# Kernel tuning notes

Measured on AMD Instinct MI355X. Metric: run time of the kernel, lower is better.

Reference implementation:

```python
import jax, jax.numpy as jnp
import numpy as np

N = 40000          # nodes
E = 640000         # edges (avg degree 16)
D = 128            # in_channels == out_channels
G = 8              # graphs
NPG = N // G       # nodes per graph
EPS = 1e-6
SLOPE = 0.01       # torch LeakyReLU default


def leaky(x):
    return jnp.where(x >= 0, x, SLOPE * x)


def setup_inputs() -> dict:
    key = jax.random.key(0)
    ks = jax.random.split(key, 8)
    x = jax.random.normal(ks[0], (N, D), dtype=jnp.float32)
    edge_index = jax.random.randint(ks[1], (2, E), 0, N, dtype=jnp.int32)
    w = jax.random.uniform(ks[2], (E, 1), dtype=jnp.float32)
    batch = jnp.repeat(jnp.arange(G, dtype=jnp.int32), NPG)
    batch_num = jnp.full((G,), NPG, dtype=jnp.int32)
    s = 1.0 / np.sqrt(D)
    W1 = jax.random.uniform(ks[3], (D, D), jnp.float32, -s, s)
    W2 = jax.random.uniform(ks[4], (D, D), jnp.float32, -s, s)
    Wo = jax.random.uniform(ks[5], (D, D), jnp.float32, -s, s)
    Wn = jax.random.uniform(ks[6], (D, D), jnp.float32, -s, s)
    gamma = jnp.ones((D,), jnp.float32)
    beta = jnp.zeros((D,), jnp.float32)
    return {"x": x, "edge_index": edge_index, "w": w, "batch": batch,
            "batch_num": batch_num, "W1": W1, "W2": W2, "Wo": Wo, "Wn": Wn,
            "gamma": gamma, "beta": beta}


def reference(x, edge_index, w, batch, batch_num, W1, W2, Wo, Wn, gamma, beta):
    # mlp_x (dropout in eval mode => identity)
    h = leaky(x @ W1) @ W2                                    # [N, D]
    # gather -> scale -> scatter-sum -> activate
    xj = w * h[edge_index[1]]                                 # [E, D]
    xn = leaky(jax.ops.segment_sum(xj, edge_index[0], num_segments=N))
    out = h @ Wo + xn @ Wn                                    # [N, D]
    # GraphNorm: per-graph mean and unbiased std (torch_scatter defaults)
    cnt = batch_num.astype(jnp.float32)[:, None]              # [G, 1]
    mu = jax.ops.segment_sum(out, batch, num_segments=G) / cnt
    diff = out - mu[batch]
    var = jax.ops.segment_sum(diff * diff, batch, num_segments=G) / (cnt - 1.0)
    sigma = jnp.sqrt(var)
    return diff / (sigma[batch] + EPS) * gamma + beta
```

## Files before the change

kernel.cpp:

```cpp
#include <hip/hip_runtime.h>
#include <hip/hip_bf16.h>

#define D 128
#define NN 40000
#define EE 640000
#define GG 8
#define NPG 5000
#define CSUB 16
#define NBKT 8
#define OVCAP 4095
#define REP 32

using short8 = __attribute__((ext_vector_type(8))) short;
using f32x4 = __attribute__((ext_vector_type(4))) float;

__device__ __forceinline__ float lrelu(float v) { return v >= 0.f ? v : 0.01f * v; }

__device__ __forceinline__ ushort f2bf(float f) {
    union { float f; uint u; } c; c.f = f;
    return (ushort)((c.u + 0x7FFFu + ((c.u >> 16) & 1u)) >> 16);
}
__device__ __forceinline__ float bf2f_lo(uint u) { union { uint u; float f; } c; c.u = u << 16; return c.f; }
__device__ __forceinline__ float bf2f_hi(uint u) { union { uint u; float f; } c; c.u = u & 0xFFFF0000u; return c.f; }

__global__ __launch_bounds__(256) void prep_k(const float* __restrict__ W1,
                                              const float* __restrict__ W2,
                                              const float* __restrict__ Wo,
                                              const float* __restrict__ Wn,
                                              short* __restrict__ WT,
                                              uint4* __restrict__ zbase, int zlen16) {
    const int b = blockIdx.x;
    if (b < 4) {
        const float* W = b == 0 ? W1 : b == 1 ? W2 : b == 2 ? Wo : Wn;
        short* T = WT + b * (D * D);
#pragma unroll 4
        for (int i = 0; i < 64; ++i) {
            int flat = threadIdx.x + i * 256;
            int k = flat >> 7, n = flat & 127;
            T[n * D + k] = (short)f2bf(W[flat]);
        }
    } else {
        int idx = (b - 4) * 256 + threadIdx.x;
        if (idx < zlen16) zbase[idx] = uint4{0, 0, 0, 0};
    }
}

__device__ __forceinline__ void stage_B(const short* __restrict__ WT,
                                        short (*Bs)[136], int tid) {
    const uint4* bsrc = (const uint4*)WT;
#pragma unroll
    for (int i = 0; i < 8; ++i) {
        int idx = tid + i * 256;
        int flat = idx * 8;
        *(uint4*)&Bs[flat >> 7][flat & 127] = bsrc[idx];
    }
}

__device__ __forceinline__ void mfma8(const short8 (&a)[4], short (*Bs)[136],
                                      f32x4 (&acc)[8], int lrow, int kgrp) {
#pragma unroll
    for (int ks = 0; ks < 4; ++ks) {
        const int kb = ks * 32 + kgrp;
#pragma unroll
        for (int nt = 0; nt < 8; ++nt) {
            short8 b = *(const short8*)&Bs[nt * 16 + lrow][kb];
            acc[nt] = __builtin_amdgcn_mfma_f32_16x16x32_bf16(a[ks], b, acc[nt], 0, 0, 0);
        }
    }
}

__global__ __launch_bounds__(256) void mlp_k(const float* __restrict__ x,
                                             const short* __restrict__ W1T,
                                             const short* __restrict__ W2T,
                                             ushort* __restrict__ h) {
    __shared__ short Bs[128][136];
    __shared__ short tw[4][16][136];
    const int tid = threadIdx.x;
    const int wv = tid >> 6, lane = tid & 63;
    const int lrow = lane & 15, kgrp = (lane >> 4) * 8;
    const int m0 = wv * 16;
    const int arow = blockIdx.x * 64;
    short8 a[4];
#pragma unroll
    for (int ks = 0; ks < 4; ++ks) {
        const float* xp = &x[(size_t)(arow + m0 + lrow) * D + ks * 32 + kgrp];
        const float4 u0 = *(const float4*)xp;
        const float4 u1 = *(const float4*)(xp + 4);
        short8 aa;
        aa[0] = (short)f2bf(u0.x); aa[1] = (short)f2bf(u0.y);
        aa[2] = (short)f2bf(u0.z); aa[3] = (short)f2bf(u0.w);
        aa[4] = (short)f2bf(u1.x); aa[5] = (short)f2bf(u1.y);
        aa[6] = (short)f2bf(u1.z); aa[7] = (short)f2bf(u1.w);
        a[ks] = aa;
    }
    stage_B(W1T, Bs, tid);
    __syncthreads();
    f32x4 acc[8] = {};
    mfma8(a, Bs, acc, lrow, kgrp);
    const int c0 = lane & 15;
    const int rg = (lane >> 4) * 4;
#pragma unroll
    for (int nt = 0; nt < 8; ++nt)
#pragma unroll
        for (int r = 0; r < 4; ++r)
            tw[wv][rg + r][nt * 16 + c0] = (short)f2bf(lrelu(acc[nt][r]));
    __syncthreads();
    stage_B(W2T, Bs, tid);
#pragma unroll
    for (int ks = 0; ks < 4; ++ks)
        a[ks] = *(const short8*)&tw[wv][lrow][ks * 32 + kgrp];
#pragma unroll
    for (int nt = 0; nt < 8; ++nt) acc[nt] = f32x4{0.f, 0.f, 0.f, 0.f};
    __syncthreads();
    mfma8(a, Bs, acc, lrow, kgrp);
#pragma unroll
    for (int nt = 0; nt < 8; ++nt)
#pragma unroll
        for (int r = 0; r < 4; ++r)
            h[(size_t)(arow + m0 + rg + r) * D + nt * 16 + c0] = f2bf(acc[nt][r]);
}

__global__ __launch_bounds__(256) void fill_k(const int* __restrict__ ei,
                                              const float* __restrict__ w,
                                              int* __restrict__ deg8,
                                              int2* __restrict__ csr,
                                              int* __restrict__ ov) {
    const int t = blockIdx.x * 256 + threadIdx.x;
    const int e0 = t * 4;
    const int kbase = (t & 1) * 4;
    const int4 dst = *(const int4*)&ei[e0];
    const int4 src = *(const int4*)&ei[EE + e0];
    const float4 wv = *(const float4*)&w[e0];
    const int ds[4] = {dst.x, dst.y, dst.z, dst.w};
    const int sr[4] = {src.x, src.y, src.z, src.w};
    const float wf[4] = {wv.x, wv.y, wv.z, wv.w};
    int pos[4];
#pragma unroll
    for (int j = 0; j < 4; ++j)
        pos[j] = atomicAdd(&deg8[ds[j] * NBKT + kbase + j], 1);
#pragma unroll
    for (int j = 0; j < 4; ++j) {
        if (pos[j] < CSUB) {
            csr[(size_t)ds[j] * (NBKT * CSUB) + (kbase + j) * CSUB + pos[j]] =
                make_int2(sr[j], __float_as_int(wf[j]));
        } else {
            const int oi = atomicAdd(&ov[0], 1);
            if (oi < OVCAP) ov[1 + oi] = e0 + j;
        }
    }
}

__global__ __launch_bounds__(256) void gather_k(const ushort* __restrict__ h,
                                                const int* __restrict__ deg8,
                                                const int2* __restrict__ csr,
                                                const int* __restrict__ ei,
                                                const float* __restrict__ w,
                                                const int* __restrict__ ov,
                                                ushort* __restrict__ xnact) {
    const int n = blockIdx.x * 16 + (threadIdx.x >> 4);
    const int lane = threadIdx.x & 15;
    const int4 da = *(const int4*)&deg8[n * NBKT];
    const int4 db = *(const int4*)&deg8[n * NBKT + 4];
    const int b0 = min(da.x, CSUB);
    const int b1 = b0 + min(da.y, CSUB);
    const int b2 = b1 + min(da.z, CSUB);
    const int b3 = b2 + min(da.w, CSUB);
    const int b4 = b3 + min(db.x, CSUB);
    const int b5 = b4 + min(db.y, CSUB);
    const int b6 = b5 + min(db.z, CSUB);
    const int total = b6 + min(db.w, CSUB);
    const int2* row = csr + (size_t)n * (NBKT * CSUB);
    auto slot = [&](int jj) -> int {
        return jj < b0 ? jj
             : jj < b1 ? jj - b0 + 16
             : jj < b2 ? jj - b1 + 32
             : jj < b3 ? jj - b2 + 48
             : jj < b4 ? jj - b3 + 64
             : jj < b5 ? jj - b4 + 80
             : jj < b6 ? jj - b5 + 96
             :           jj - b6 + 112;
    };
    float acc[8] = {};
    int j = 0;
#define GBODY(NB)                                                              \
    {                                                                          \
        int2 p[NB]; uint4 v[NB];                                               \
        _Pragma("unroll") for (int t = 0; t < NB; ++t) p[t] = row[slot(j + t)];\
        _Pragma("unroll") for (int t = 0; t < NB; ++t)                         \
            v[t] = *((const uint4*)(h + (size_t)p[t].x * D) + lane);           \
        _Pragma("unroll") for (int t = 0; t < NB; ++t) {                       \
            const float wv = __int_as_float(p[t].y);                           \
            acc[0] += wv * bf2f_lo(v[t].x); acc[1] += wv * bf2f_hi(v[t].x);    \
            acc[2] += wv * bf2f_lo(v[t].y); acc[3] += wv * bf2f_hi(v[t].y);    \
            acc[4] += wv * bf2f_lo(v[t].z); acc[5] += wv * bf2f_hi(v[t].z);    \
            acc[6] += wv * bf2f_lo(v[t].w); acc[7] += wv * bf2f_hi(v[t].w);    \
        }                                                                      \
        j += NB;                                                               \
    }
    while (j + 16 <= total) GBODY(16)
    while (j + 4 <= total) GBODY(4)
    for (; j < total; ++j) {
        const int2 p = row[slot(j)];
        const uint4 v = *((const uint4*)(h + (size_t)p.x * D) + lane);
        const float wv = __int_as_float(p.y);
        acc[0] += wv * bf2f_lo(v.x); acc[1] += wv * bf2f_hi(v.x);
        acc[2] += wv * bf2f_lo(v.y); acc[3] += wv * bf2f_hi(v.y);
        acc[4] += wv * bf2f_lo(v.z); acc[5] += wv * bf2f_hi(v.z);
        acc[6] += wv * bf2f_lo(v.w); acc[7] += wv * bf2f_hi(v.w);
    }
#undef GBODY
    if (da.x > CSUB || da.y > CSUB || da.z > CSUB || da.w > CSUB ||
        db.x > CSUB || db.y > CSUB || db.z > CSUB || db.w > CSUB) {
        const int cnt = min(ov[0], OVCAP);
        for (int i = 0; i < cnt; ++i) {
            const int e = ov[1 + i];
            if (ei[e] == n) {
                const float wv = w[e];
                const uint4 v = *((const uint4*)(h + (size_t)ei[EE + e] * D) + lane);
                acc[0] += wv * bf2f_lo(v.x); acc[1] += wv * bf2f_hi(v.x);
                acc[2] += wv * bf2f_lo(v.y); acc[3] += wv * bf2f_hi(v.y);
                acc[4] += wv * bf2f_lo(v.z); acc[5] += wv * bf2f_hi(v.z);
                acc[6] += wv * bf2f_lo(v.w); acc[7] += wv * bf2f_hi(v.w);
            }
        }
    }
    uint4 st;
    st.x = (uint)f2bf(lrelu(acc[0])) | ((uint)f2bf(lrelu(acc[1])) << 16);
    st.y = (uint)f2bf(lrelu(acc[2])) | ((uint)f2bf(lrelu(acc[3])) << 16);
    st.z = (uint)f2bf(lrelu(acc[4])) | ((uint)f2bf(lrelu(acc[5])) << 16);
    st.w = (uint)f2bf(lrelu(acc[6])) | ((uint)f2bf(lrelu(acc[7])) << 16);
    *((uint4*)(xnact + (size_t)n * D) + lane) = st;
}

__global__ __launch_bounds__(256) void mmstats_k(const ushort* __restrict__ h,
                                                 const short* __restrict__ WoT,
                                                 const ushort* __restrict__ xa,
                                                 const short* __restrict__ WnT,
                                                 float* __restrict__ out,
                                                 float* __restrict__ statsR) {
    __shared__ short Bs[128][136];
    __shared__ float ls[2][16][132];
    const int tid = threadIdx.x;
    const int wv = tid >> 6, lane = tid & 63;
    const int lrow = lane & 15, kgrp = (lane >> 4) * 8;
    const int m0 = wv * 16;
    const int arow = blockIdx.x * 64;
    short8 a[4];
#pragma unroll
    for (int ks = 0; ks < 4; ++ks)
        a[ks] = *(const short8*)&h[(size_t)(arow + m0 + lrow) * D + ks * 32 + kgrp];
    stage_B(WoT, Bs, tid);
    __syncthreads();
    f32x4 acc[8] = {};
    mfma8(a, Bs, acc, lrow, kgrp);
#pragma unroll
    for (int ks = 0; ks < 4; ++ks)
        a[ks] = *(const short8*)&xa[(size_t)(arow + m0 + lrow) * D + ks * 32 + kgrp];
    __syncthreads();
    stage_B(WnT, Bs, tid);
    __syncthreads();
    mfma8(a, Bs, acc, lrow, kgrp);
    const int c0 = lane & 15;
    const int rg = (lane >> 4) * 4;
    const int li = wv * 4 + (lane >> 4);
#pragma unroll
    for (int nt = 0; nt < 8; ++nt) {
        float s = 0.f, q = 0.f;
#pragma unroll
        for (int r = 0; r < 4; ++r) {
            const float v = acc[nt][r];
            out[(size_t)(arow + m0 + rg + r) * D + nt * 16 + c0] = v;
            s += v; q += v * v;
        }
        ls[0][li][nt * 16 + c0] = s;
        ls[1][li][nt * 16 + c0] = q;
    }
    __syncthreads();
    if (tid < 128) {
        const int g0 = arow / NPG;
        const int gsplit = (g0 + 1) * NPG - arow;
        float s0 = 0.f, q0 = 0.f, s1 = 0.f, q1 = 0.f;
#pragma unroll
        for (int i = 0; i < 16; ++i) {
            const float sv = ls[0][i][tid];
            const float qv = ls[1][i][tid];
            if (i * 4 >= gsplit) { s1 += sv; q1 += qv; }
            else { s0 += sv; q0 += qv; }
        }
        const int rep = blockIdx.x & (REP - 1);
        float* S = &statsR[(size_t)rep * (2 * GG * D) + 0 * GG * D + g0 * D + tid];
        float* Q = &statsR[(size_t)rep * (2 * GG * D) + 1 * GG * D + g0 * D + tid];
        atomicAdd(S, s0);
        atomicAdd(Q, q0);
        if (gsplit < 64) { atomicAdd(S + D, s1); atomicAdd(Q + D, q1); }
    }
}

__global__ __launch_bounds__(256) void reduce_k(const float* __restrict__ statsR,
                                                float* __restrict__ statsF) {
    const int idx = blockIdx.x * 256 + threadIdx.x;
    float s = 0.f;
#pragma unroll
    for (int rep = 0; rep < REP; ++rep) s += statsR[rep * (2 * GG * D) + idx];
    statsF[idx] = s;
}

__global__ __launch_bounds__(256) void norm_k(float* __restrict__ out,
                                              const float* __restrict__ statsF,
                                              const float* __restrict__ gamma,
                                              const float* __restrict__ beta) {
    const int i4 = blockIdx.x * 256 + threadIdx.x;
    const int row = i4 >> 5;
    const int g = row / NPG;
    const int d0 = (i4 & 31) * 4;
    float4 v = *((float4*)out + i4);
    const float4 s4 = *(const float4*)&statsF[g * D + d0];
    const float4 q4 = *(const float4*)&statsF[GG * D + g * D + d0];
    const float4 g4 = *(const float4*)&gamma[d0];
    const float4 b4 = *(const float4*)&beta[d0];
    const float inv = 1.f / (float)NPG;
    const float invm1 = 1.f / (float)(NPG - 1);
    float mu, var, sg;
    mu = s4.x * inv; var = (q4.x - s4.x * mu) * invm1; sg = sqrtf(fmaxf(var, 0.f));
    v.x = (v.x - mu) / (sg + 1e-6f) * g4.x + b4.x;
    mu = s4.y * inv; var = (q4.y - s4.y * mu) * invm1; sg = sqrtf(fmaxf(var, 0.f));
    v.y = (v.y - mu) / (sg + 1e-6f) * g4.y + b4.y;
    mu = s4.z * inv; var = (q4.z - s4.z * mu) * invm1; sg = sqrtf(fmaxf(var, 0.f));
    v.z = (v.z - mu) / (sg + 1e-6f) * g4.z + b4.z;
    mu = s4.w * inv; var = (q4.w - s4.w * mu) * invm1; sg = sqrtf(fmaxf(var, 0.f));
    v.w = (v.w - mu) / (sg + 1e-6f) * g4.w + b4.w;
    *((float4*)out + i4) = v;
}

extern "C" void kernel_launch(void* const* d_in, const int* in_sizes, int n_in,
                              void* d_out, int out_size, void* d_ws, size_t ws_size,
                              hipStream_t stream) {
    const float* x = (const float*)d_in[0];
    const int* ei = (const int*)d_in[1];
    const float* w = (const float*)d_in[2];
    const float* W1 = (const float*)d_in[5];
    const float* W2 = (const float*)d_in[6];
    const float* Wo = (const float*)d_in[7];
    const float* Wn = (const float*)d_in[8];
    const float* gamma = (const float*)d_in[9];
    const float* beta = (const float*)d_in[10];
    float* out = (float*)d_out;

    char* ws = (char*)d_ws;
    const size_t BF16MAT = (size_t)NN * D * 2;
    size_t off = 0;
    ushort* h = (ushort*)(ws + off);      off += BF16MAT;
    ushort* xnact = (ushort*)(ws + off);  off += BF16MAT;
    const size_t ZOFF = off;
    float* statsR = (float*)(ws + off);   off += (size_t)REP * 2 * GG * D * 4;
    float* statsF = (float*)(ws + off);   off += 2 * GG * D * 4;
    int* deg8 = (int*)(ws + off);         off += (size_t)NN * NBKT * 4;
    int* ov = (int*)(ws + off);           off += (1 + OVCAP) * 4;
    const int ZLEN16 = (int)((off - ZOFF) / 16);
    short* WT = (short*)(ws + off);       off += 4 * (size_t)D * D * 2;
    int2* csr = (int2*)(ws + off);

    prep_k<<<4 + (ZLEN16 + 255) / 256, 256, 0, stream>>>(W1, W2, Wo, Wn, WT,
                                                         (uint4*)(ws + ZOFF), ZLEN16);
    mlp_k<<<NN / 64, 256, 0, stream>>>(x, WT, WT + D * D, h);
    fill_k<<<EE / (256 * 4), 256, 0, stream>>>(ei, w, deg8, csr, ov);
    gather_k<<<NN / 16, 256, 0, stream>>>(h, deg8, csr, ei, w, ov, xnact);
    mmstats_k<<<NN / 64, 256, 0, stream>>>(h, WT + 2 * D * D, xnact, WT + 3 * D * D, out, statsR);
    reduce_k<<<(2 * GG * D) / 256, 256, 0, stream>>>(statsR, statsF);
    norm_k<<<(NN * D / 4) / 256, 256, 0, stream>>>(out, statsF, gamma, beta);
}
```

Measured before the change: 214.2 us.

## Fuse MLP and CSR fill into one launch and shrink bucket layout to four

Merges the MLP kernel and the edge bucket-fill kernel into a single launch, with blocks split by index, so the independent fill work overlaps with the MLP matmuls and one launch is saved. The per-node bucket count drops from eight to four, giving a 64-slot CSR row, and degree counters move to a structure-of-arrays layout. This shrinks the slot-lookup chain in the gather and the counter footprint. The gather loop now runs in batches of 8 rather than 16. The cost is more atomic contention per bucket and more edges spilling into the overflow list when a node's bucket degree exceeds 16.

```diff
diff --git a/kernel.cpp b/kernel.cpp
--- a/kernel.cpp
+++ b/kernel.cpp
@@ -7,7 +7,6 @@
 #define GG 8
 #define NPG 5000
 #define CSUB 16
-#define NBKT 8
 #define OVCAP 4095
 #define REP 32
 
@@ -69,89 +68,87 @@
     }
 }
 
-__global__ __launch_bounds__(256) void mlp_k(const float* __restrict__ x,
-                                             const short* __restrict__ W1T,
-                                             const short* __restrict__ W2T,
-                                             ushort* __restrict__ h) {
+__global__ __launch_bounds__(256) void mlpfill_k(const float* __restrict__ x,
+                                                 const short* __restrict__ W1T,
+                                                 const short* __restrict__ W2T,
+                                                 ushort* __restrict__ h,
+                                                 const int* __restrict__ ei,
+                                                 const float* __restrict__ w,
+                                                 int* __restrict__ deg4,
+                                                 int2* __restrict__ csr,
+                                                 int* __restrict__ ov) {
     __shared__ short Bs[128][136];
     __shared__ short tw[4][16][136];
     const int tid = threadIdx.x;
-    const int wv = tid >> 6, lane = tid & 63;
-    const int lrow = lane & 15, kgrp = (lane >> 4) * 8;
-    const int m0 = wv * 16;
-    const int arow = blockIdx.x * 64;
-    short8 a[4];
-#pragma unroll
-    for (int ks = 0; ks < 4; ++ks) {
-        const float* xp = &x[(size_t)(arow + m0 + lrow) * D + ks * 32 + kgrp];
-        const float4 u0 = *(const float4*)xp;
-        const float4 u1 = *(const float4*)(xp + 4);
-        short8 aa;
-        aa[0] = (short)f2bf(u0.x); aa[1] = (short)f2bf(u0.y);
-        aa[2] = (short)f2bf(u0.z); aa[3] = (short)f2bf(u0.w);
-        aa[4] = (short)f2bf(u1.x); aa[5] = (short)f2bf(u1.y);
-        aa[6] = (short)f2bf(u1.z); aa[7] = (short)f2bf(u1.w);
-        a[ks] = aa;
-    }
-    stage_B(W1T, Bs, tid);
-    __syncthreads();
-    f32x4 acc[8] = {};
-    mfma8(a, Bs, acc, lrow, kgrp);
-    const int c0 = lane & 15;
-    const int rg = (lane >> 4) * 4;
-#pragma unroll
-    for (int nt = 0; nt < 8; ++nt)
-#pragma unroll
-        for (int r = 0; r < 4; ++r)
-            tw[wv][rg + r][nt * 16 + c0] = (short)f2bf(lrelu(acc[nt][r]));
-    __syncthreads();
-    stage_B(W2T, Bs, tid);
-#pragma unroll
-    for (int ks = 0; ks < 4; ++ks)
-        a[ks] = *(const short8*)&tw[wv][lrow][ks * 32 + kgrp];
-#pragma unroll
-    for (int nt = 0; nt < 8; ++nt) acc[nt] = f32x4{0.f, 0.f, 0.f, 0.f};
-    __syncthreads();
-    mfma8(a, Bs, acc, lrow, kgrp);
-#pragma unroll
-    for (int nt = 0; nt < 8; ++nt)
-#pragma unroll
-        for (int r = 0; r < 4; ++r)
-            h[(size_t)(arow + m0 + rg + r) * D + nt * 16 + c0] = f2bf(acc[nt][r]);
-}
-
-__global__ __launch_bounds__(256) void fill_k(const int* __restrict__ ei,
-                                              const float* __restrict__ w,
-                                              int* __restrict__ deg8,
-                                              int2* __restrict__ csr,
-                                              int* __restrict__ ov) {
-    const int t = blockIdx.x * 256 + threadIdx.x;
-    const int e0 = t * 4;
-    const int kbase = (t & 1) * 4;
-    const int4 dst = *(const int4*)&ei[e0];
-    const int4 src = *(const int4*)&ei[EE + e0];
-    const float4 wv = *(const float4*)&w[e0];
-    const int ds[4] = {dst.x, dst.y, dst.z, dst.w};
-    const int sr[4] = {src.x, src.y, src.z, src.w};
-    const float wf[4] = {wv.x, wv.y, wv.z, wv.w};
-    int pos[4];
-#pragma unroll
-    for (int j = 0; j < 4; ++j)
-        pos[j] = atomicAdd(&deg8[ds[j] * NBKT + kbase + j], 1);
-#pragma unroll
-    for (int j = 0; j < 4; ++j) {
-        if (pos[j] < CSUB) {
-            csr[(size_t)ds[j] * (NBKT * CSUB) + (kbase + j) * CSUB + pos[j]] =
-                make_int2(sr[j], __float_as_int(wf[j]));
-        } else {
-            const int oi = atomicAdd(&ov[0], 1);
-            if (oi < OVCAP) ov[1 + oi] = e0 + j;
+    if (blockIdx.x < NN / 64) {
+        const int wv = tid >> 6, lane = tid & 63;
+        const int lrow = lane & 15, kgrp = (lane >> 4) * 8;
+        const int m0 = wv * 16;
+        const int arow = blockIdx.x * 64;
+        short8 a[4];
+#pragma unroll
+        for (int ks = 0; ks < 4; ++ks) {
+            const float* xp = &x[(size_t)(arow + m0 + lrow) * D + ks * 32 + kgrp];
+            const float4 u0 = *(const float4*)xp;
+            const float4 u1 = *(const float4*)(xp + 4);
+            short8 aa;
+            aa[0] = (short)f2bf(u0.x); aa[1] = (short)f2bf(u0.y);
+            aa[2] = (short)f2bf(u0.z); aa[3] = (short)f2bf(u0.w);
+            aa[4] = (short)f2bf(u1.x); aa[5] = (short)f2bf(u1.y);
+            aa[6] = (short)f2bf(u1.z); aa[7] = (short)f2bf(u1.w);
+            a[ks] = aa;
+        }
+        stage_B(W1T, Bs, tid);
+        __syncthreads();
+        f32x4 acc[8] = {};
+        mfma8(a, Bs, acc, lrow, kgrp);
+        const int c0 = lane & 15;
+        const int rg = (lane >> 4) * 4;
+#pragma unroll
+        for (int nt = 0; nt < 8; ++nt)
+#pragma unroll
+            for (int r = 0; r < 4; ++r)
+                tw[wv][rg + r][nt * 16 + c0] = (short)f2bf(lrelu(acc[nt][r]));
+        __syncthreads();
+        stage_B(W2T, Bs, tid);
+#pragma unroll
+        for (int ks = 0; ks < 4; ++ks)
+            a[ks] = *(const short8*)&tw[wv][lrow][ks * 32 + kgrp];
+#pragma unroll
+        for (int nt = 0; nt < 8; ++nt) acc[nt] = f32x4{0.f, 0.f, 0.f, 0.f};
+        __syncthreads();
+        mfma8(a, Bs, acc, lrow, kgrp);
+#pragma unroll
+        for (int nt = 0; nt < 8; ++nt)
+#pragma unroll
+            for (int r = 0; r < 4; ++r)
+                h[(size_t)(arow + m0 + rg + r) * D + nt * 16 + c0] = f2bf(acc[nt][r]);
+    } else {
+        const int t = (blockIdx.x - NN / 64) * 256 + tid;
+        const int e0 = t * 4;
+        const int4 dst = *(const int4*)&ei[e0];
+        const int4 src = *(const int4*)&ei[EE + e0];
+        const float4 wv4 = *(const float4*)&w[e0];
+        const int ds[4] = {dst.x, dst.y, dst.z, dst.w};
+        const int sr[4] = {src.x, src.y, src.z, src.w};
+        const float wf[4] = {wv4.x, wv4.y, wv4.z, wv4.w};
+        int pos[4];
+#pragma unroll
+        for (int k = 0; k < 4; ++k) pos[k] = atomicAdd(&deg4[k * NN + ds[k]], 1);
+#pragma unroll
+        for (int k = 0; k < 4; ++k) {
+            if (pos[k] < CSUB) {
+                csr[(size_t)ds[k] * 64 + k * CSUB + pos[k]] = make_int2(sr[k], __float_as_int(wf[k]));
+            } else {
+                const int oi = atomicAdd(&ov[0], 1);
+                if (oi < OVCAP) ov[1 + oi] = e0 + k;
+            }
         }
     }
 }
 
 __global__ __launch_bounds__(256) void gather_k(const ushort* __restrict__ h,
-                                                const int* __restrict__ deg8,
+                                                const int* __restrict__ deg4,
                                                 const int2* __restrict__ csr,
                                                 const int* __restrict__ ei,
                                                 const float* __restrict__ w,
@@ -159,48 +156,66 @@
                                                 ushort* __restrict__ xnact) {
     const int n = blockIdx.x * 16 + (threadIdx.x >> 4);
     const int lane = threadIdx.x & 15;
-    const int4 da = *(const int4*)&deg8[n * NBKT];
-    const int4 db = *(const int4*)&deg8[n * NBKT + 4];
-    const int b0 = min(da.x, CSUB);
-    const int b1 = b0 + min(da.y, CSUB);
-    const int b2 = b1 + min(da.z, CSUB);
-    const int b3 = b2 + min(da.w, CSUB);
-    const int b4 = b3 + min(db.x, CSUB);
-    const int b5 = b4 + min(db.y, CSUB);
-    const int b6 = b5 + min(db.z, CSUB);
-    const int total = b6 + min(db.w, CSUB);
-    const int2* row = csr + (size_t)n * (NBKT * CSUB);
-    auto slot = [&](int jj) -> int {
-        return jj < b0 ? jj
-             : jj < b1 ? jj - b0 + 16
-             : jj < b2 ? jj - b1 + 32
-             : jj < b3 ? jj - b2 + 48
-             : jj < b4 ? jj - b3 + 64
-             : jj < b5 ? jj - b4 + 80
-             : jj < b6 ? jj - b5 + 96
-             :           jj - b6 + 112;
-    };
+    const int d0 = deg4[0 * NN + n], d1 = deg4[1 * NN + n];
+    const int d2 = deg4[2 * NN + n], d3 = deg4[3 * NN + n];
+    const int c0 = min(d0, CSUB), c1 = min(d1, CSUB);
+    const int c2 = min(d2, CSUB), c3 = min(d3, CSUB);
+    const int t0 = c0, t1 = t0 + c1, t2 = t1 + c2;
+    const int total = t2 + c3;
+    const int2* row = csr + (size_t)n * 64;
     float acc[8] = {};
     int j = 0;
-#define GBODY(NB)                                                              \
-    {                                                                          \
-        int2 p[NB]; uint4 v[NB];                                               \
-        _Pragma("unroll") for (int t = 0; t < NB; ++t) p[t] = row[slot(j + t)];\
-        _Pragma("unroll") for (int t = 0; t < NB; ++t)                         \
-            v[t] = *((const uint4*)(h + (size_t)p[t].x * D) + lane);           \
-        _Pragma("unroll") for (int t = 0; t < NB; ++t) {                       \
-            const float wv = __int_as_float(p[t].y);                           \
-            acc[0] += wv * bf2f_lo(v[t].x); acc[1] += wv * bf2f_hi(v[t].x);    \
-            acc[2] += wv * bf2f_lo(v[t].y); acc[3] += wv * bf2f_hi(v[t].y);    \
-            acc[4] += wv * bf2f_lo(v[t].z); acc[5] += wv * bf2f_hi(v[t].z);    \
-            acc[6] += wv * bf2f_lo(v[t].w); acc[7] += wv * bf2f_hi(v[t].w);    \
-        }                                                                      \
-        j += NB;                                                               \
-    }
-    while (j + 16 <= total) GBODY(16)
-    while (j + 4 <= total) GBODY(4)
+    for (; j + 8 <= total; j += 8) {
+        int2 p[8]; uint4 v[8];
+#pragma unroll
+        for (int t = 0; t < 8; ++t) {
+            const int jj = j + t;
+            const int s = jj < t0 ? jj
+                        : jj < t1 ? jj - t0 + CSUB
+                        : jj < t2 ? jj - t1 + 2 * CSUB
+                                  : jj - t2 + 3 * CSUB;
+            p[t] = row[s];
+        }
+#pragma unroll
+        for (int t = 0; t < 8; ++t) v[t] = *((const uint4*)(h + (size_t)p[t].x * D) + lane);
+#pragma unroll
+        for (int t = 0; t < 8; ++t) {
+            const float wv = __int_as_float(p[t].y);
+            acc[0] += wv * bf2f_lo(v[t].x); acc[1] += wv * bf2f_hi(v[t].x);
+            acc[2] += wv * bf2f_lo(v[t].y); acc[3] += wv * bf2f_hi(v[t].y);
+            acc[4] += wv * bf2f_lo(v[t].z); acc[5] += wv * bf2f_hi(v[t].z);
+            acc[6] += wv * bf2f_lo(v[t].w); acc[7] += wv * bf2f_hi(v[t].w);
+        }
+    }
+    if (j + 4 <= total) {
+        int2 p[4]; uint4 v[4];
+#pragma unroll
+        for (int t = 0; t < 4; ++t) {
+            const int jj = j + t;
+            const int s = jj < t0 ? jj
+                        : jj < t1 ? jj - t0 + CSUB
+                        : jj < t2 ? jj - t1 + 2 * CSUB
+                                  : jj - t2 + 3 * CSUB;
+            p[t] = row[s];
+        }
+#pragma unroll
+        for (int t = 0; t < 4; ++t) v[t] = *((const uint4*)(h + (size_t)p[t].x * D) + lane);
+#pragma unroll
+        for (int t = 0; t < 4; ++t) {
+            const float wv = __int_as_float(p[t].y);
+            acc[0] += wv * bf2f_lo(v[t].x); acc[1] += wv * bf2f_hi(v[t].x);
+            acc[2] += wv * bf2f_lo(v[t].y); acc[3] += wv * bf2f_hi(v[t].y);
+            acc[4] += wv * bf2f_lo(v[t].z); acc[5] += wv * bf2f_hi(v[t].z);
+            acc[6] += wv * bf2f_lo(v[t].w); acc[7] += wv * bf2f_hi(v[t].w);
+        }
+        j += 4;
+    }
     for (; j < total; ++j) {
-        const int2 p = row[slot(j)];
+        const int s = j < t0 ? j
+                    : j < t1 ? j - t0 + CSUB
+                    : j < t2 ? j - t1 + 2 * CSUB
+                             : j - t2 + 3 * CSUB;
+        const int2 p = row[s];
         const uint4 v = *((const uint4*)(h + (size_t)p.x * D) + lane);
         const float wv = __int_as_float(p.y);
         acc[0] += wv * bf2f_lo(v.x); acc[1] += wv * bf2f_hi(v.x);
@@ -208,9 +223,7 @@
         acc[4] += wv * bf2f_lo(v.z); acc[5] += wv * bf2f_hi(v.z);
         acc[6] += wv * bf2f_lo(v.w); acc[7] += wv * bf2f_hi(v.w);
     }
-#undef GBODY
-    if (da.x > CSUB || da.y > CSUB || da.z > CSUB || da.w > CSUB ||
-        db.x > CSUB || db.y > CSUB || db.z > CSUB || db.w > CSUB) {
+    if (d0 > CSUB || d1 > CSUB || d2 > CSUB || d3 > CSUB) {
         const int cnt = min(ov[0], OVCAP);
         for (int i = 0; i < cnt; ++i) {
             const int e = ov[1 + i];
@@ -354,7 +367,7 @@
     const size_t ZOFF = off;
     float* statsR = (float*)(ws + off);   off += (size_t)REP * 2 * GG * D * 4;
     float* statsF = (float*)(ws + off);   off += 2 * GG * D * 4;
-    int* deg8 = (int*)(ws + off);         off += (size_t)NN * NBKT * 4;
+    int* deg4 = (int*)(ws + off);         off += (size_t)NN * 4 * 4;
     int* ov = (int*)(ws + off);           off += (1 + OVCAP) * 4;
     const int ZLEN16 = (int)((off - ZOFF) / 16);
     short* WT = (short*)(ws + off);       off += 4 * (size_t)D * D * 2;
@@ -362,9 +375,9 @@
 
     prep_k<<<4 + (ZLEN16 + 255) / 256, 256, 0, stream>>>(W1, W2, Wo, Wn, WT,
                                                          (uint4*)(ws + ZOFF), ZLEN16);
-    mlp_k<<<NN / 64, 256, 0, stream>>>(x, WT, WT + D * D, h);
-    fill_k<<<EE / (256 * 4), 256, 0, stream>>>(ei, w, deg8, csr, ov);
-    gather_k<<<NN / 16, 256, 0, stream>>>(h, deg8, csr, ei, w, ov, xnact);
+    mlpfill_k<<<2 * (NN / 64), 256, 0, stream>>>(x, WT, WT + D * D, h,
+                                                 ei, w, deg4, csr, ov);
+    gather_k<<<NN / 16, 256, 0, stream>>>(h, deg4, csr, ei, w, ov, xnact);
     mmstats_k<<<NN / 64, 256, 0, stream>>>(h, WT + 2 * D * D, xnact, WT + 3 * D * D, out, statsR);
     reduce_k<<<(2 * GG * D) / 256, 256, 0, stream>>>(statsR, statsF);
     norm_k<<<(NN * D / 4) / 256, 256, 0, stream>>>(out, statsF, gamma, beta);
```

Result: faster. 193.9 us (-9.5%).
